# Kernel tuning notes

Hardware: AMD Instinct MI355X
Metric: run time of the kernel (lower is better)

## Reference

```python
import jax, jax.numpy as jnp
import numpy as np

B, S, D, H, V, N_SHARDS, CAP = 4, 512, 512, 8, 32000, 64, 128
HD = D // H


def _layernorm(x, g, b, eps=1e-5):
    mu = x.mean(-1, keepdims=True)
    var = ((x - mu) ** 2).mean(-1, keepdims=True)
    return (x - mu) * jax.lax.rsqrt(var + eps) * g + b


def setup_inputs() -> dict:
    key = jax.random.key(0)
    ks = jax.random.split(key, 16)
    s = 0.02
    return {
        'input_ids': jax.random.randint(ks[0], (B, S), 0, V, dtype=jnp.int32),
        'emb': jax.random.normal(ks[1], (V, D), jnp.float32) * s,
        'Wq': jax.random.normal(ks[2], (D, D), jnp.float32) * s,
        'Wk': jax.random.normal(ks[3], (D, D), jnp.float32) * s,
        'Wv': jax.random.normal(ks[4], (D, D), jnp.float32) * s,
        'Wo': jax.random.normal(ks[5], (D, D), jnp.float32) * s,
        'ln_g': jnp.ones((D,), jnp.float32),
        'ln_b': jnp.zeros((D,), jnp.float32),
        'W_router': jax.random.normal(ks[6], (D, N_SHARDS), jnp.float32),
        'mem_keys': jax.random.normal(ks[7], (N_SHARDS, CAP, D), jnp.float32) * s,
        'mem_values': jax.random.normal(ks[8], (N_SHARDS, CAP, D), jnp.float32) * s,
        'Wg_c': jax.random.normal(ks[9], (D, D), jnp.float32) * s,
        'Wg_m': jax.random.normal(ks[10], (D, D), jnp.float32) * s,
        'bg': jnp.zeros((D,), jnp.float32),
        'Wd': jax.random.normal(ks[11], (D, V), jnp.float32) * s,
        'bd': jnp.zeros((V,), jnp.float32),
        'top_k': 4,
    }


def reference(input_ids, emb, Wq, Wk, Wv, Wo, ln_g, ln_b, W_router,
              mem_keys, mem_values, Wg_c, Wg_m, bg, Wd, bd, top_k):
    # --- encode_context: embedding + causal MHA block (ContextSynthesizer) ---
    x = emb[input_ids]                                   # [B,S,D]
    q = (x @ Wq).reshape(B, S, H, HD)
    k = (x @ Wk).reshape(B, S, H, HD)
    v = (x @ Wv).reshape(B, S, H, HD)
    att = jnp.einsum('bqhd,bkhd->bhqk', q, k) / jnp.sqrt(jnp.float32(HD))
    causal = jnp.tril(jnp.ones((S, S), bool))
    att = jnp.where(causal[None, None], att, jnp.finfo(att.dtype).min)
    att = jax.nn.softmax(att, axis=-1)
    o = jnp.einsum('bhqk,bkhd->bqhd', att, v).reshape(B, S, D) @ Wo
    ctx = _layernorm(x + o, ln_g, ln_b)                  # [B,S,D]

    # --- LSHRouter: hyperplane projection -> shard id per token ---
    routes = jnp.argmax(ctx @ W_router, axis=-1)         # [B,S] int

    # --- MemoryShardStore.query, batched: per-token routed shard top-k read ---
    keys_g = mem_keys[routes]                            # [B,S,CAP,D] irregular gather
    scores = jnp.einsum('bscd,bsd->bsc', keys_g, ctx)    # [B,S,CAP]
    top_v, top_i = jax.lax.top_k(scores, top_k)          # [B,S,k]
    w = jax.nn.softmax(top_v, axis=-1)
    vals = mem_values[routes[:, :, None], top_i]         # [B,S,k,D]
    memory_stream = jnp.einsum('bsk,bskd->bsd', w, vals)

    # --- GatedMemoryFusion ---
    gate = jax.nn.sigmoid(ctx @ Wg_c + memory_stream @ Wg_m + bg)
    fused = gate * ctx + (1.0 - gate) * memory_stream

    # --- decoder; payload bias is zero (store holds no sequence_chunk records) ---
    logits = fused @ Wd + bd                             # [B,S,V]
    return logits
```

## Files before the change

### kernel.cpp

```cpp
#include <hip/hip_runtime.h>

typedef unsigned short u16;
typedef float f32x4 __attribute__((ext_vector_type(4)));
typedef short short8 __attribute__((ext_vector_type(8)));
typedef __bf16 bf16x8 __attribute__((ext_vector_type(8)));

#define B_  4
#define S_  512
#define D_  512
#define H_  8
#define HD_ 64
#define V_  32000
#define NSHARD_ 64
#define CAP_ 128
#define TOK_ (B_ * S_)

__device__ __forceinline__ float bf2f(u16 u) { return __uint_as_float(((unsigned)u) << 16); }
__device__ __forceinline__ u16 f2bf(float f) {
  unsigned u = __float_as_uint(f);
  u += 0x7FFFu + ((u >> 16) & 1u);
  return (u16)(u >> 16);
}

__device__ __forceinline__ f32x4 mfma16(short8 a, short8 b, f32x4 c) {
  return __builtin_amdgcn_mfma_f32_16x16x32_bf16(
      __builtin_bit_cast(bf16x8, a), __builtin_bit_cast(bf16x8, b), c, 0, 0, 0);
}

__device__ __forceinline__ void load_lds16(const void* g, void* l) {
  __builtin_amdgcn_global_load_lds(
      (const __attribute__((address_space(1))) void*)g,
      (__attribute__((address_space(3))) void*)l, 16, 0, 0);
}

template<int NS, bool ACC, int OM, bool CKLIM>
__global__ __launch_bounds__(256) void gemm_bt(
    const u16* __restrict__ Ah, const u16* __restrict__ Al, int ldA, long sA1, long sA2,
    const u16* __restrict__ Bh, const u16* __restrict__ Bl, int ldB, long sB1, long sB2,
    void* __restrict__ C0, void* __restrict__ C1, int ldC, long sC1, long sC2,
    int K, int z2n, float alpha)
{
  __shared__ u16 AsH[64 * 64];
  __shared__ u16 BsH[64 * 64];
  __shared__ u16 AsL[(NS == 3) ? 64 * 64 : 8];
  __shared__ u16 BsL[(NS == 3) ? 64 * 64 : 8];

  const int n0 = blockIdx.x * 64;
  const int m0 = blockIdx.y * 64;

  const int z = blockIdx.z;
  const int z1 = z / z2n, z2 = z - z1 * z2n;
  const long baseA = (long)z1 * sA1 + (long)z2 * sA2;
  const long baseB = (long)z1 * sB1 + (long)z2 * sB2;
  const long baseC = (long)z1 * sC1 + (long)z2 * sC2;

  const int tid = threadIdx.x;
  const int lane = tid & 63;
  const int w = tid >> 6;
  const int wm = (w >> 1) * 32, wn = (w & 1) * 32;
  const int fr = lane & 15, kg = lane >> 4;

  const int srow = lane >> 3;
  const int schunk = (lane & 7) ^ srow;

  const u16* gAh = Ah + baseA + (long)(m0 + w * 16 + srow) * ldA + schunk * 8;
  const u16* gBh = Bh + baseB + (long)(n0 + w * 16 + srow) * ldB + schunk * 8;
  const u16* gAl = (NS == 3) ? (Al + baseA + (long)(m0 + w * 16 + srow) * ldA + schunk * 8) : nullptr;
  const u16* gBl = (NS == 3) ? (Bl + baseB + (long)(n0 + w * 16 + srow) * ldB + schunk * 8) : nullptr;
  u16* lAh = &AsH[(w * 16) * 64];
  u16* lBh = &BsH[(w * 16) * 64];
  u16* lAl = &AsL[(NS == 3) ? (w * 16) * 64 : 0];
  u16* lBl = &BsL[(NS == 3) ? (w * 16) * 64 : 0];

  const int kmax = CKLIM ? (m0 + 64) : K;

  f32x4 acc[2][2] = {};

  for (int k0 = 0; k0 < kmax; k0 += 64) {
    load_lds16(gAh + k0, lAh);
    load_lds16(gAh + k0 + 8 * ldA, lAh + 8 * 64);
    load_lds16(gBh + k0, lBh);
    load_lds16(gBh + k0 + 8 * ldB, lBh + 8 * 64);
    if (NS == 3) {
      load_lds16(gAl + k0, lAl);
      load_lds16(gAl + k0 + 8 * ldA, lAl + 8 * 64);
      load_lds16(gBl + k0, lBl);
      load_lds16(gBl + k0 + 8 * ldB, lBl + 8 * 64);
    }
    __syncthreads();

    short8 ah[2][2], bh[2][2], al[2][2], bl[2][2];
#pragma unroll
    for (int mi = 0; mi < 2; ++mi) {
      int row = wm + mi * 16 + fr;
#pragma unroll
      for (int ks = 0; ks < 2; ++ks) {
        int idx = row * 64 + ((ks * 32 + kg * 8) ^ ((fr & 7) << 3));
        ah[mi][ks] = *(const short8*)&AsH[idx];
        if (NS == 3) al[mi][ks] = *(const short8*)&AsL[idx];
      }
    }
#pragma unroll
    for (int ni = 0; ni < 2; ++ni) {
      int row = wn + ni * 16 + fr;
#pragma unroll
      for (int ks = 0; ks < 2; ++ks) {
        int idx = row * 64 + ((ks * 32 + kg * 8) ^ ((fr & 7) << 3));
        bh[ni][ks] = *(const short8*)&BsH[idx];
        if (NS == 3) bl[ni][ks] = *(const short8*)&BsL[idx];
      }
    }
#pragma unroll
    for (int ks = 0; ks < 2; ++ks)
#pragma unroll
      for (int mi = 0; mi < 2; ++mi)
#pragma unroll
        for (int ni = 0; ni < 2; ++ni) {
          acc[mi][ni] = mfma16(ah[mi][ks], bh[ni][ks], acc[mi][ni]);
          if (NS == 3) {
            acc[mi][ni] = mfma16(ah[mi][ks], bl[ni][ks], acc[mi][ni]);
            acc[mi][ni] = mfma16(al[mi][ks], bh[ni][ks], acc[mi][ni]);
          }
        }
    __syncthreads();
  }

#pragma unroll
  for (int mi = 0; mi < 2; ++mi)
#pragma unroll
    for (int ni = 0; ni < 2; ++ni) {
      int gnc = n0 + wn + ni * 16 + fr;
#pragma unroll
      for (int r = 0; r < 4; ++r) {
        int gm = m0 + wm + mi * 16 + kg * 4 + r;
        float v = acc[mi][ni][r] * alpha;
        long idx = baseC + (long)gm * ldC + gnc;
        if (OM == 0) {
          float* C = (float*)C0;
          C[idx] = ACC ? (C[idx] + v) : v;
        } else {
          u16 h = f2bf(v);
          ((u16*)C0)[idx] = h;
          ((u16*)C1)[idx] = f2bf(v - bf2f(h));
        }
      }
    }
}

__global__ __launch_bounds__(256) void gate_gemm_k(
    const u16* __restrict__ Ah, const u16* __restrict__ Bh,
    const float* __restrict__ bgp, const float* __restrict__ ctxf,
    const float* __restrict__ msf, u16* __restrict__ fused)
{
  __shared__ u16 AsH[64 * 64];
  __shared__ u16 BsH[64 * 64];

  const int n0 = blockIdx.x * 64;
  const int m0 = blockIdx.y * 64;
  const int tid = threadIdx.x;
  const int lane = tid & 63;
  const int w = tid >> 6;
  const int wm = (w >> 1) * 32, wn = (w & 1) * 32;
  const int fr = lane & 15, kg = lane >> 4;
  const int srow = lane >> 3;
  const int schunk = (lane & 7) ^ srow;

  const u16* gAh = Ah + (long)(m0 + w * 16 + srow) * 1024 + schunk * 8;
  const u16* gBh = Bh + (long)(n0 + w * 16 + srow) * 1024 + schunk * 8;
  u16* lAh = &AsH[(w * 16) * 64];
  u16* lBh = &BsH[(w * 16) * 64];

  f32x4 acc[2][2] = {};

  for (int k0 = 0; k0 < 1024; k0 += 64) {
    load_lds16(gAh + k0, lAh);
    load_lds16(gAh + k0 + 8 * 1024, lAh + 8 * 64);
    load_lds16(gBh + k0, lBh);
    load_lds16(gBh + k0 + 8 * 1024, lBh + 8 * 64);
    __syncthreads();

    short8 ah[2][2], bh[2][2];
#pragma unroll
    for (int mi = 0; mi < 2; ++mi) {
      int row = wm + mi * 16 + fr;
#pragma unroll
      for (int ks = 0; ks < 2; ++ks)
        ah[mi][ks] = *(const short8*)&AsH[row * 64 +
                         ((ks * 32 + kg * 8) ^ ((fr & 7) << 3))];
    }
#pragma unroll
    for (int ni = 0; ni < 2; ++ni) {
      int row = wn + ni * 16 + fr;
#pragma unroll
      for (int ks = 0; ks < 2; ++ks)
        bh[ni][ks] = *(const short8*)&BsH[row * 64 +
                         ((ks * 32 + kg * 8) ^ ((fr & 7) << 3))];
    }
#pragma unroll
    for (int ks = 0; ks < 2; ++ks)
#pragma unroll
      for (int mi = 0; mi < 2; ++mi)
#pragma unroll
        for (int ni = 0; ni < 2; ++ni)
          acc[mi][ni] = mfma16(ah[mi][ks], bh[ni][ks], acc[mi][ni]);
    __syncthreads();
  }

#pragma unroll
  for (int mi = 0; mi < 2; ++mi)
#pragma unroll
    for (int ni = 0; ni < 2; ++ni) {
      int gnc = n0 + wn + ni * 16 + fr;
      float bv = bgp[gnc];
#pragma unroll
      for (int r = 0; r < 4; ++r) {
        int gm = m0 + wm + mi * 16 + kg * 4 + r;
        long idx = (long)gm * D_ + gnc;
        float g = 1.f / (1.f + expf(-(acc[mi][ni][r] + bv)));
        fused[idx] = f2bf(g * ctxf[idx] + (1.f - g) * msf[idx]);
      }
    }
}

__global__ __launch_bounds__(256) void qkt_k(
    const u16* __restrict__ qkvh, const u16* __restrict__ qkvl,
    float* __restrict__ att)
{
  const int n0 = blockIdx.x * 64;
  const int m0 = blockIdx.y * 64;
  if (n0 > m0 + 63) return;
  const int z = blockIdx.z;
  const int b = z >> 3, h = z & 7;
  const long qbase = (long)b * 512 * 1536 + h * 64;
  const long kbase = qbase + 512;
  const long cbase = (long)z * 512 * 512;

  const int tid = threadIdx.x;
  const int lane = tid & 63;
  const int w = tid >> 6;
  const int wm = (w >> 1) * 32, wn = (w & 1) * 32;
  const int fr = lane & 15, kg = lane >> 4;

  short8 ah[2][2], al[2][2], bh[2][2], bl[2][2];
#pragma unroll
  for (int mi = 0; mi < 2; ++mi)
#pragma unroll
    for (int ks = 0; ks < 2; ++ks) {
      long ra = qbase + (long)(m0 + wm + mi * 16 + fr) * 1536 + ks * 32 + kg * 8;
      ah[mi][ks] = *(const short8*)(qkvh + ra);
      al[mi][ks] = *(const short8*)(qkvl + ra);
    }
#pragma unroll
  for (int ni = 0; ni < 2; ++ni)
#pragma unroll
    for (int ks = 0; ks < 2; ++ks) {
      long rb = kbase + (long)(n0 + wn + ni * 16 + fr) * 1536 + ks * 32 + kg * 8;
      bh[ni][ks] = *(const short8*)(qkvh + rb);
      bl[ni][ks] = *(const short8*)(qkvl + rb);
    }

  f32x4 acc[2][2] = {};
#pragma unroll
  for (int ks = 0; ks < 2; ++ks)
#pragma unroll
    for (int mi = 0; mi < 2; ++mi)
#pragma unroll
      for (int ni = 0; ni < 2; ++ni) {
        acc[mi][ni] = mfma16(ah[mi][ks], bh[ni][ks], acc[mi][ni]);
        acc[mi][ni] = mfma16(ah[mi][ks], bl[ni][ks], acc[mi][ni]);
        acc[mi][ni] = mfma16(al[mi][ks], bh[ni][ks], acc[mi][ni]);
      }

#pragma unroll
  for (int mi = 0; mi < 2; ++mi)
#pragma unroll
    for (int ni = 0; ni < 2; ++ni) {
      int gnc = n0 + wn + ni * 16 + fr;
#pragma unroll
      for (int r = 0; r < 4; ++r) {
        int gm = m0 + wm + mi * 16 + kg * 4 + r;
        att[cbase + (long)gm * 512 + gnc] = acc[mi][ni][r] * 0.125f;
      }
    }
}

__global__ __launch_bounds__(512, 4) void logits_gemm_bk32_k(
    const u16* __restrict__ A, const u16* __restrict__ Bt,
    const float* __restrict__ bias, float* __restrict__ C)
{
  __shared__ u16 As[2][256 * 32];
  __shared__ u16 Bs[2][128 * 32];

  const int id = blockIdx.x;
  const int swz = (id & 7) * 250 + (id >> 3);
  const int m0 = (swz & 7) * 256;
  const int n0 = (swz >> 3) * 128;

  const int tid = threadIdx.x;
  const int lane = tid & 63;
  const int wid = tid >> 6;
  const int wr = wid >> 1;
  const int wc = wid & 1;
  const int fr = lane & 15, kg = lane >> 4;
  const int srow = lane >> 2;
  const int schunk = (lane & 3) ^ (srow & 3);

  f32x4 acc[4][4] = {};
  short8 a[4], b[4];

  auto stage = [&](int kt) {
    const int buf = kt & 1;
    const long kc = (long)kt * 32 + schunk * 8;
    load_lds16(A + (long)(m0 + wid * 16 + srow) * D_ + kc,
               &As[buf][(wid * 16) * 32]);
    load_lds16(A + (long)(m0 + 128 + wid * 16 + srow) * D_ + kc,
               &As[buf][(128 + wid * 16) * 32]);
    load_lds16(Bt + (long)(n0 + wid * 16 + srow) * D_ + kc,
               &Bs[buf][(wid * 16) * 32]);
  };
  auto readfrags = [&](int buf) {
#pragma unroll
    for (int mi = 0; mi < 4; ++mi) {
      int row = wr * 64 + mi * 16 + fr;
      a[mi] = *(const short8*)&As[buf][row * 32 + ((kg ^ (row & 3)) * 8)];
    }
#pragma unroll
    for (int ni = 0; ni < 4; ++ni) {
      int row = wc * 64 + ni * 16 + fr;
      b[ni] = *(const short8*)&Bs[buf][row * 32 + ((kg ^ (row & 3)) * 8)];
    }
  };

  stage(0);
  stage(1);

  for (int t = 0; t < 16; ++t) {
    __builtin_amdgcn_sched_barrier(0);
    if (t < 15) { asm volatile("s_waitcnt vmcnt(3)" ::: "memory"); }
    else        { asm volatile("s_waitcnt vmcnt(0)" ::: "memory"); }
    __builtin_amdgcn_s_barrier();
    __builtin_amdgcn_sched_barrier(0);

    readfrags(t & 1);
    asm volatile("s_waitcnt lgkmcnt(0)" ::: "memory");
    __builtin_amdgcn_sched_barrier(0);
    __builtin_amdgcn_s_barrier();
    __builtin_amdgcn_sched_barrier(0);

    if (t + 2 < 16) stage(t + 2);

    __builtin_amdgcn_sched_barrier(0);
    __builtin_amdgcn_s_setprio(1);
#pragma unroll
    for (int mi = 0; mi < 4; ++mi)
#pragma unroll
      for (int ni = 0; ni < 4; ++ni)
        acc[mi][ni] = mfma16(a[mi], b[ni], acc[mi][ni]);
    __builtin_amdgcn_s_setprio(0);
    __builtin_amdgcn_sched_barrier(0);
  }

#pragma unroll
  for (int ni = 0; ni < 4; ++ni) {
    int gnc = n0 + wc * 64 + ni * 16 + fr;
    float bv = bias[gnc];
#pragma unroll
    for (int mi = 0; mi < 4; ++mi)
#pragma unroll
      for (int r = 0; r < 4; ++r) {
        int gm = m0 + wr * 64 + mi * 16 + kg * 4 + r;
        __builtin_nontemporal_store(acc[mi][ni][r] + bv, &C[(long)gm * V_ + gnc]);
      }
  }
}

__global__ __launch_bounds__(256) void prep_weights_k(
    const float* __restrict__ Wq, const float* __restrict__ Wk,
    const float* __restrict__ Wv, const float* __restrict__ Wo,
    const float* __restrict__ Wgc, const float* __restrict__ Wgm,
    const float* __restrict__ Wd,
    u16* __restrict__ wqkvTh, u16* __restrict__ wqkvTl,
    u16* __restrict__ woTh, u16* __restrict__ woTl,
    u16* __restrict__ wgT, u16* __restrict__ wdT)
{
  const int bid = blockIdx.x;
  const float* W; u16 *oh, *ol = nullptr;
  int ldw, ldo, koff = 0, nb, kb;
  bool LO = false;
  if (bid < 384) {
    const int w = bid >> 6, tt = bid & 63;
    nb = tt & 7; kb = tt >> 3;
    ldw = 512; ldo = 512;
    switch (w) {
      case 0: W = Wq;  oh = wqkvTh;               ol = wqkvTl;               LO = true; break;
      case 1: W = Wk;  oh = wqkvTh + 512 * 512;   ol = wqkvTl + 512 * 512;   LO = true; break;
      case 2: W = Wv;  oh = wqkvTh + 2 * 512 * 512; ol = wqkvTl + 2 * 512 * 512; LO = true; break;
      case 3: W = Wo;  oh = woTh;                 ol = woTl;                 LO = true; break;
      case 4: W = Wgc; oh = wgT; ldo = 1024; break;
      default: W = Wgm; oh = wgT; ldo = 1024; koff = 512; break;
    }
  } else {
    const int tt = bid - 384;
    nb = tt % 500; kb = tt / 500;
    W = Wd; ldw = V_; ldo = 512; oh = wdT;
  }
  const int n0 = nb * 64, k0 = kb * 64;
  const int tid = threadIdx.x;
  __shared__ float t[64][65];
  {
    const int kk = tid >> 4;
    const int c4 = (tid & 15) * 4;
#pragma unroll
    for (int i = 0; i < 4; ++i) {
      f32x4 v = *(const f32x4*)(W + (long)(k0 + kk + i * 16) * ldw + n0 + c4);
      t[kk + i * 16][c4] = v[0];
      t[kk + i * 16][c4 + 1] = v[1];
      t[kk + i * 16][c4 + 2] = v[2];
      t[kk + i * 16][c4 + 3] = v[3];
    }
  }
  __syncthreads();
  {
    const int chunk = tid & 7;
    const int nn = tid >> 3;
#pragma unroll
    for (int j = 0; j < 2; ++j) {
      int n = nn + j * 32;
      u16 hbuf[8], lbuf[8];
#pragma unroll
      for (int e = 0; e < 8; ++e) {
        float fv = t[chunk * 8 + e][n];
        u16 h = f2bf(fv);
        hbuf[e] = h;
        lbuf[e] = f2bf(fv - bf2f(h));
      }
      long ob = (long)(n0 + n) * ldo + koff + k0 + chunk * 8;
      *(short8*)(oh + ob) = *(short8*)hbuf;
      if (LO) *(short8*)(ol + ob) = *(short8*)lbuf;
    }
  }
}

__global__ __launch_bounds__(256) void v_transpose_k(
    const u16* __restrict__ qh, const u16* __restrict__ ql,
    u16* __restrict__ vTh, u16* __restrict__ vTl)
{
  __shared__ u16 th[64][68];
  __shared__ u16 tl[64][68];
  const int z = blockIdx.y;
  const int b = z >> 3, h = z & 7;
  const int s0 = blockIdx.x * 64;
  const long ibase = ((long)(b * 512 + s0)) * 1536 + 1024 + h * 64;
  const int tid = threadIdx.x;
  {
    const int sr = tid >> 2;
    const int c8 = (tid & 3) * 16;
    const long src = ibase + (long)sr * 1536 + c8;
    *(short8*)&th[sr][c8]     = *(const short8*)(qh + src);
    *(short8*)&th[sr][c8 + 8] = *(const short8*)(qh + src + 8);
    *(short8*)&tl[sr][c8]     = *(const short8*)(ql + src);
    *(short8*)&tl[sr][c8 + 8] = *(const short8*)(ql + src + 8);
  }
  __syncthreads();
  {
    const int dr = tid >> 2;
    const int s8 = (tid & 3) * 16;
    u16 oh[16], ol[16];
#pragma unroll
    for (int j = 0; j < 16; ++j) { oh[j] = th[s8 + j][dr]; ol[j] = tl[s8 + j][dr]; }
    long ob = (long)z * 64 * 512 + (long)dr * 512 + s0 + s8;
    *(short8*)(vTh + ob)     = *(short8*)&oh[0];
    *(short8*)(vTh + ob + 8) = *(short8*)&oh[8];
    *(short8*)(vTl + ob)     = *(short8*)&ol[0];
    *(short8*)(vTl + ob + 8) = *(short8*)&ol[8];
  }
}

__global__ __launch_bounds__(128) void embed_k(const int* __restrict__ ids,
                                               const float* __restrict__ emb,
                                               float* __restrict__ x,
                                               u16* __restrict__ xh,
                                               u16* __restrict__ xl) {
  const int t = blockIdx.x;
  const long id = ids[t];
  const int c = threadIdx.x * 4;
  f32x4 v = *(const f32x4*)(emb + id * (long)D_ + c);
  *(f32x4*)(x + (long)t * D_ + c) = v;
  u16 hh[4], ll[4];
#pragma unroll
  for (int j = 0; j < 4; ++j) {
    u16 h = f2bf(v[j]);
    hh[j] = h;
    ll[j] = f2bf(v[j] - bf2f(h));
  }
  *(unsigned long long*)(xh + (long)t * D_ + c) = *(unsigned long long*)hh;
  *(unsigned long long*)(xl + (long)t * D_ + c) = *(unsigned long long*)ll;
}

__global__ __launch_bounds__(64) void softmax_causal_k(
    const float* __restrict__ att, u16* __restrict__ ph, u16* __restrict__ pl) {
  const int row = blockIdx.x;
  const int i = row & 511;
  const long base = (long)row << 9;
  const float* p = att + base;
  const int lane = threadIdx.x;
  const int c0 = lane * 8;
  float v[8];
  float m = -3.4e38f;
  if (c0 <= i) {
    f32x4 a = *(const f32x4*)(p + c0);
    f32x4 b2 = *(const f32x4*)(p + c0 + 4);
#pragma unroll
    for (int j = 0; j < 8; ++j) {
      float x = (j < 4) ? a[j] : b2[j - 4];
      x = (c0 + j <= i) ? x : -3.4e38f;
      v[j] = x;
      m = fmaxf(m, x);
    }
  } else {
#pragma unroll
    for (int j = 0; j < 8; ++j) v[j] = 0.f;
  }
#pragma unroll
  for (int off = 32; off; off >>= 1) m = fmaxf(m, __shfl_xor(m, off));
  float s = 0.f;
  if (c0 <= i) {
#pragma unroll
    for (int j = 0; j < 8; ++j) {
      float e = (c0 + j <= i) ? expf(v[j] - m) : 0.f;
      v[j] = e;
      s += e;
    }
  }
#pragma unroll
  for (int off = 32; off; off >>= 1) s += __shfl_xor(s, off);
  float inv = 1.f / s;
  if (c0 <= (i | 63)) {
    u16 hh[8], ll[8];
#pragma unroll
    for (int j = 0; j < 8; ++j) {
      float e = (c0 <= i) ? v[j] * inv : 0.f;
      u16 h = f2bf(e);
      hh[j] = h;
      ll[j] = f2bf(e - bf2f(h));
    }
    *(short8*)(ph + base + c0) = *(short8*)hh;
    *(short8*)(pl + base + c0) = *(short8*)ll;
  }
}

__global__ __launch_bounds__(128) void ln_route_k(
    const float* __restrict__ x, const float* __restrict__ proj,
    const float* __restrict__ g, const float* __restrict__ b,
    const float* __restrict__ Wr, const float* __restrict__ keys,
    const float* __restrict__ valsm,
    float* __restrict__ ctxf, u16* __restrict__ catA, float* __restrict__ msf)
{
  const int t = blockIdx.x;
  const int tid = threadIdx.x;
  __shared__ float sctx[D_];
  __shared__ float red2[4];
  __shared__ float spart[CAP_];
  __shared__ float sred2[2][64];
  __shared__ int s_route;
  __shared__ int sidx[4];
  __shared__ float sw[4];

  const int c = tid * 4;
  f32x4 xv = *(const f32x4*)(x + (long)t * D_ + c);
  f32x4 pv = *(const f32x4*)(proj + (long)t * D_ + c);
  float v0 = xv[0] + pv[0], v1 = xv[1] + pv[1];
  float v2 = xv[2] + pv[2], v3 = xv[3] + pv[3];
  float s = v0 + v1 + v2 + v3;
  float q = v0 * v0 + v1 * v1 + v2 * v2 + v3 * v3;
#pragma unroll
  for (int off = 32; off; off >>= 1) { s += __shfl_xor(s, off); q += __shfl_xor(q, off); }
  const int wave = tid >> 6, lane = tid & 63;
  if (lane == 0) { red2[wave] = s; red2[2 + wave] = q; }
  __syncthreads();
  s = red2[0] + red2[1];
  q = red2[2] + red2[3];
  float mu = s * (1.f / 512.f);
  float var = q * (1.f / 512.f) - mu * mu;
  float rs = rsqrtf(var + 1e-5f);
  f32x4 gv = *(const f32x4*)(g + c);
  f32x4 bv = *(const f32x4*)(b + c);
  f32x4 of;
  of[0] = (v0 - mu) * rs * gv[0] + bv[0];
  of[1] = (v1 - mu) * rs * gv[1] + bv[1];
  of[2] = (v2 - mu) * rs * gv[2] + bv[2];
  of[3] = (v3 - mu) * rs * gv[3] + bv[3];
  *(f32x4*)(ctxf + (long)t * D_ + c) = of;
  ((f32x4*)sctx)[tid] = of;
  {
    u16 hh[4];
#pragma unroll
    for (int j = 0; j < 4; ++j) hh[j] = f2bf(of[j]);
    *(unsigned long long*)(catA + (long)t * 1024 + c) = *(unsigned long long*)hh;
  }
  __syncthreads();

  {
    const int cc = tid & 63, half = tid >> 6;
    float accr = 0.f;
    const float* cp = sctx + half * 256;
    const float* wp = Wr + (long)(half * 256) * NSHARD_ + cc;
    for (int d = 0; d < 256; ++d) accr += cp[d] * wp[(long)d * NSHARD_];
    sred2[half][cc] = accr;
  }
  __syncthreads();
  if (tid < 64) {
    float v = sred2[0][tid] + sred2[1][tid];
    int idx = tid;
#pragma unroll
    for (int off = 32; off; off >>= 1) {
      float ov = __shfl_xor(v, off);
      int oi = __shfl_xor(idx, off);
      if (ov > v || (ov == v && oi < idx)) { v = ov; idx = oi; }
    }
    if (tid == 0) s_route = idx;
  }
  __syncthreads();
  const int route = s_route;

  {
    const float* krow = keys + ((long)route * CAP_ + tid) * D_;
    float sc = 0.f;
    for (int d0 = 0; d0 < D_; d0 += 4) {
      f32x4 kv = *(const f32x4*)(krow + d0);
      sc += sctx[d0] * kv[0] + sctx[d0 + 1] * kv[1] +
            sctx[d0 + 2] * kv[2] + sctx[d0 + 3] * kv[3];
    }
    spart[tid] = sc;
  }
  __syncthreads();

  for (int rep = 0; rep < 4; ++rep) {
    if (tid < 64) {
      float v1r = spart[tid]; int i1 = tid;
      float v2r = spart[tid + 64]; int i2 = tid + 64;
      float v; int idx;
      if (v2r > v1r) { v = v2r; idx = i2; } else { v = v1r; idx = i1; }
#pragma unroll
      for (int off = 32; off; off >>= 1) {
        float ov = __shfl_xor(v, off);
        int oi = __shfl_xor(idx, off);
        if (ov > v || (ov == v && oi < idx)) { v = ov; idx = oi; }
      }
      if (tid == 0) { sidx[rep] = idx; sw[rep] = v; spart[idx] = -3.4e38f; }
    }
    __syncthreads();
  }

  float w0 = sw[0], w1 = sw[1], w2 = sw[2], w3 = sw[3];
  float mx = fmaxf(fmaxf(w0, w1), fmaxf(w2, w3));
  float e0 = expf(w0 - mx), e1 = expf(w1 - mx), e2 = expf(w2 - mx), e3 = expf(w3 - mx);
  float inv = 1.f / (e0 + e1 + e2 + e3);
  float wk[4] = {e0 * inv, e1 * inv, e2 * inv, e3 * inv};

  float a0 = 0, a1 = 0, a2 = 0, a3 = 0;
#pragma unroll
  for (int k = 0; k < 4; ++k) {
    const float* vr = valsm + ((long)route * CAP_ + sidx[k]) * D_ + c;
    f32x4 vv = *(const f32x4*)vr;
    float w = wk[k];
    a0 += w * vv[0]; a1 += w * vv[1]; a2 += w * vv[2]; a3 += w * vv[3];
  }
  f32x4 om; om[0] = a0; om[1] = a1; om[2] = a2; om[3] = a3;
  *(f32x4*)(msf + (long)t * D_ + c) = om;
  u16 oh[4];
  oh[0] = f2bf(a0); oh[1] = f2bf(a1); oh[2] = f2bf(a2); oh[3] = f2bf(a3);
  *(unsigned long long*)(catA + (long)t * 1024 + 512 + c) =
      *(unsigned long long*)oh;
}

extern "C" void kernel_launch(void* const* d_in, const int* in_sizes, int n_in,
                              void* d_out, int out_size, void* d_ws, size_t ws_size,
                              hipStream_t stream) {
  const int*   ids  = (const int*)d_in[0];
  const float* emb  = (const float*)d_in[1];
  const float* Wq   = (const float*)d_in[2];
  const float* Wk   = (const float*)d_in[3];
  const float* Wv   = (const float*)d_in[4];
  const float* Wo   = (const float*)d_in[5];
  const float* ln_g = (const float*)d_in[6];
  const float* ln_b = (const float*)d_in[7];
  const float* Wr   = (const float*)d_in[8];
  const float* mk   = (const float*)d_in[9];
  const float* mv   = (const float*)d_in[10];
  const float* Wgc  = (const float*)d_in[11];
  const float* Wgm  = (const float*)d_in[12];
  const float* bg   = (const float*)d_in[13];
  const float* Wd   = (const float*)d_in[14];
  const float* bd   = (const float*)d_in[15];
  float* out = (float*)d_out;

  char* ws = (char*)d_ws;
  size_t off = 0;
  auto alloc = [&](size_t bytes) -> void* {
    void* p = ws + off;
    off += (bytes + 255) & ~(size_t)255;
    return p;
  };
  float* x      = (float*)alloc((size_t)TOK_ * D_ * 4);
  u16*   xh     = (u16*)  alloc((size_t)TOK_ * D_ * 2);
  u16*   xl     = (u16*)  alloc((size_t)TOK_ * D_ * 2);
  u16*   wqkvTh = (u16*)  alloc((size_t)3 * D_ * D_ * 2);
  u16*   wqkvTl = (u16*)  alloc((size_t)3 * D_ * D_ * 2);
  u16*   woTh   = (u16*)  alloc((size_t)D_ * D_ * 2);
  u16*   woTl   = (u16*)  alloc((size_t)D_ * D_ * 2);
  u16*   wgT    = (u16*)  alloc((size_t)D_ * 1024 * 2);
  u16*   wdT    = (u16*)  alloc((size_t)D_ * V_ * 2);
  u16*   qkvh   = (u16*)  alloc((size_t)TOK_ * 3 * D_ * 2);
  u16*   qkvl   = (u16*)  alloc((size_t)TOK_ * 3 * D_ * 2);
  u16*   vTh    = (u16*)  alloc((size_t)B_ * H_ * HD_ * S_ * 2);
  u16*   vTl    = (u16*)  alloc((size_t)B_ * H_ * HD_ * S_ * 2);
  float* att    = (float*)alloc((size_t)B_ * H_ * S_ * S_ * 4);
  u16*   ph     = (u16*)  alloc((size_t)B_ * H_ * S_ * S_ * 2);
  u16*   pl     = (u16*)  alloc((size_t)B_ * H_ * S_ * S_ * 2);
  u16*   oh     = (u16*)  alloc((size_t)TOK_ * D_ * 2);
  u16*   ol     = (u16*)  alloc((size_t)TOK_ * D_ * 2);
  float* proj   = (float*)alloc((size_t)TOK_ * D_ * 4);
  float* ctxf   = (float*)alloc((size_t)TOK_ * D_ * 4);
  u16*   catA   = (u16*)  alloc((size_t)TOK_ * 1024 * 2);
  float* msf    = (float*)alloc((size_t)TOK_ * D_ * 4);
  u16*   fused  = (u16*)  alloc((size_t)TOK_ * D_ * 2);

  prep_weights_k<<<4384, 256, 0, stream>>>(
      Wq, Wk, Wv, Wo, Wgc, Wgm, Wd,
      wqkvTh, wqkvTl, woTh, woTl, wgT, wdT);

  embed_k<<<TOK_, 128, 0, stream>>>(ids, emb, x, xh, xl);

  {
    dim3 g(1536 / 64, TOK_ / 64, 1);
    gemm_bt<3, false, 1, false><<<g, 256, 0, stream>>>(
        xh, xl, D_, 0, 0, wqkvTh, wqkvTl, D_, 0, 0,
        qkvh, qkvl, 1536, 0, 0, D_, 1, 1.f);
  }

  {
    dim3 g(S_ / 64, B_ * H_, 1);
    v_transpose_k<<<g, 256, 0, stream>>>(qkvh, qkvl, vTh, vTl);
  }

  {
    dim3 g(S_ / 64, S_ / 64, B_ * H_);
    qkt_k<<<g, 256, 0, stream>>>(qkvh, qkvl, att);
  }

  softmax_causal_k<<<B_ * H_ * S_, 64, 0, stream>>>(att, ph, pl);

  {
    dim3 g(1, S_ / 64, B_ * H_);
    gemm_bt<3, false, 1, true><<<g, 256, 0, stream>>>(
        ph, pl, S_, (long)H_ * S_ * S_, (long)S_ * S_,
        vTh, vTl, S_, (long)H_ * HD_ * S_, (long)HD_ * S_,
        oh, ol, D_, (long)S_ * D_, HD_,
        S_, H_, 1.f);
  }

  {
    dim3 g(D_ / 64, TOK_ / 64, 1);
    gemm_bt<3, false, 0, false><<<g, 256, 0, stream>>>(
        oh, ol, D_, 0, 0, woTh, woTl, D_, 0, 0,
        proj, nullptr, D_, 0, 0, D_, 1, 1.f);
  }

  ln_route_k<<<TOK_, 128, 0, stream>>>(
      x, proj, ln_g, ln_b, Wr, mk, mv, ctxf, catA, msf);

  {
    dim3 g(D_ / 64, TOK_ / 64, 1);
    gate_gemm_k<<<g, 256, 0, stream>>>(catA, wgT, bg, ctxf, msf, fused);
  }

  logits_gemm_bk32_k<<<2000, 512, 0, stream>>>(fused, wdT, bd, out);
}
```

Baseline: 299.3 us.

## Fuse embedding into weight prep and overlap Wd transpose with QK^T kernel

Merges the embedding gather into the small weight-prep kernel, moves the large Wd transpose/bf16 conversion into extra blocks of the QK^T launch, and drops the fp32 copy of x by reconstructing it from the hi/lo bf16 split in the layernorm kernel. The intent is to cut launches, remove an fp32 write and read of x, and let the memory-bound Wd conversion run alongside the mostly idle causal QK^T grid. The risk is heterogeneous blocks unbalancing the grid, plus a tiny precision change from rebuilding x out of two bf16 halves.

Result: faster. 289.7 us (-3.2%).

```diff
diff --git a/kernel.cpp b/kernel.cpp
--- a/kernel.cpp
+++ b/kernel.cpp
@@ -4,6 +4,7 @@
 typedef float f32x4 __attribute__((ext_vector_type(4)));
 typedef short short8 __attribute__((ext_vector_type(8)));
 typedef __bf16 bf16x8 __attribute__((ext_vector_type(8)));
+typedef unsigned long long ull;
 
 #define B_  4
 #define S_  512
@@ -147,6 +148,104 @@
     }
 }
 
+__global__ __launch_bounds__(256) void qkt_wd_k(
+    const u16* __restrict__ qkvh, const u16* __restrict__ qkvl,
+    float* __restrict__ att,
+    const float* __restrict__ Wd, u16* __restrict__ wdT)
+{
+  __shared__ float t[64][65];
+  const int z = blockIdx.z;
+  const int tid = threadIdx.x;
+
+  if (z >= 32) {
+    const int tt = (z - 32) * 64 + blockIdx.y * 8 + blockIdx.x;
+    if (tt >= 4000) return;
+    const int nb = tt % 500, kb = tt / 500;
+    const int n0 = nb * 64, k0 = kb * 64;
+    {
+      const int kk = tid >> 4;
+      const int c4 = (tid & 15) * 4;
+#pragma unroll
+      for (int i = 0; i < 4; ++i) {
+        f32x4 v = *(const f32x4*)(Wd + (long)(k0 + kk + i * 16) * V_ + n0 + c4);
+        t[kk + i * 16][c4] = v[0];
+        t[kk + i * 16][c4 + 1] = v[1];
+        t[kk + i * 16][c4 + 2] = v[2];
+        t[kk + i * 16][c4 + 3] = v[3];
+      }
+    }
+    __syncthreads();
+    {
+      const int chunk = tid & 7;
+      const int nn = tid >> 3;
+#pragma unroll
+      for (int j = 0; j < 2; ++j) {
+        int n = nn + j * 32;
+        u16 hbuf[8];
+#pragma unroll
+        for (int e = 0; e < 8; ++e) hbuf[e] = f2bf(t[chunk * 8 + e][n]);
+        *(short8*)(wdT + (long)(n0 + n) * 512 + k0 + chunk * 8) = *(short8*)hbuf;
+      }
+    }
+    return;
+  }
+
+  const int n0 = blockIdx.x * 64;
+  const int m0 = blockIdx.y * 64;
+  if (n0 > m0 + 63) return;
+  const int b = z >> 3, h = z & 7;
+  const long qbase = (long)b * 512 * 1536 + h * 64;
+  const long kbase = qbase + 512;
+  const long cbase = (long)z * 512 * 512;
+
+  const int lane = tid & 63;
+  const int w = tid >> 6;
+  const int wm = (w >> 1) * 32, wn = (w & 1) * 32;
+  const int fr = lane & 15, kg = lane >> 4;
+
+  short8 ah[2][2], al[2][2], bh[2][2], bl[2][2];
+#pragma unroll
+  for (int mi = 0; mi < 2; ++mi)
+#pragma unroll
+    for (int ks = 0; ks < 2; ++ks) {
+      long ra = qbase + (long)(m0 + wm + mi * 16 + fr) * 1536 + ks * 32 + kg * 8;
+      ah[mi][ks] = *(const short8*)(qkvh + ra);
+      al[mi][ks] = *(const short8*)(qkvl + ra);
+    }
+#pragma unroll
+  for (int ni = 0; ni < 2; ++ni)
+#pragma unroll
+    for (int ks = 0; ks < 2; ++ks) {
+      long rb = kbase + (long)(n0 + wn + ni * 16 + fr) * 1536 + ks * 32 + kg * 8;
+      bh[ni][ks] = *(const short8*)(qkvh + rb);
+      bl[ni][ks] = *(const short8*)(qkvl + rb);
+    }
+
+  f32x4 acc[2][2] = {};
+#pragma unroll
+  for (int ks = 0; ks < 2; ++ks)
+#pragma unroll
+    for (int mi = 0; mi < 2; ++mi)
+#pragma unroll
+      for (int ni = 0; ni < 2; ++ni) {
+        acc[mi][ni] = mfma16(ah[mi][ks], bh[ni][ks], acc[mi][ni]);
+        acc[mi][ni] = mfma16(ah[mi][ks], bl[ni][ks], acc[mi][ni]);
+        acc[mi][ni] = mfma16(al[mi][ks], bh[ni][ks], acc[mi][ni]);
+      }
+
+#pragma unroll
+  for (int mi = 0; mi < 2; ++mi)
+#pragma unroll
+    for (int ni = 0; ni < 2; ++ni) {
+      int gnc = n0 + wn + ni * 16 + fr;
+#pragma unroll
+      for (int r = 0; r < 4; ++r) {
+        int gm = m0 + wm + mi * 16 + kg * 4 + r;
+        att[cbase + (long)gm * 512 + gnc] = acc[mi][ni][r] * 0.125f;
+      }
+    }
+}
+
 __global__ __launch_bounds__(256) void gate_gemm_k(
     const u16* __restrict__ Ah, const u16* __restrict__ Bh,
     const float* __restrict__ bgp, const float* __restrict__ ctxf,
@@ -218,68 +317,6 @@
         long idx = (long)gm * D_ + gnc;
         float g = 1.f / (1.f + expf(-(acc[mi][ni][r] + bv)));
         fused[idx] = f2bf(g * ctxf[idx] + (1.f - g) * msf[idx]);
-      }
-    }
-}
-
-__global__ __launch_bounds__(256) void qkt_k(
-    const u16* __restrict__ qkvh, const u16* __restrict__ qkvl,
-    float* __restrict__ att)
-{
-  const int n0 = blockIdx.x * 64;
-  const int m0 = blockIdx.y * 64;
-  if (n0 > m0 + 63) return;
-  const int z = blockIdx.z;
-  const int b = z >> 3, h = z & 7;
-  const long qbase = (long)b * 512 * 1536 + h * 64;
-  const long kbase = qbase + 512;
-  const long cbase = (long)z * 512 * 512;
-
-  const int tid = threadIdx.x;
-  const int lane = tid & 63;
-  const int w = tid >> 6;
-  const int wm = (w >> 1) * 32, wn = (w & 1) * 32;
-  const int fr = lane & 15, kg = lane >> 4;
-
-  short8 ah[2][2], al[2][2], bh[2][2], bl[2][2];
-#pragma unroll
-  for (int mi = 0; mi < 2; ++mi)
-#pragma unroll
-    for (int ks = 0; ks < 2; ++ks) {
-      long ra = qbase + (long)(m0 + wm + mi * 16 + fr) * 1536 + ks * 32 + kg * 8;
-      ah[mi][ks] = *(const short8*)(qkvh + ra);
-      al[mi][ks] = *(const short8*)(qkvl + ra);
-    }
-#pragma unroll
-  for (int ni = 0; ni < 2; ++ni)
-#pragma unroll
-    for (int ks = 0; ks < 2; ++ks) {
-      long rb = kbase + (long)(n0 + wn + ni * 16 + fr) * 1536 + ks * 32 + kg * 8;
-      bh[ni][ks] = *(const short8*)(qkvh + rb);
-      bl[ni][ks] = *(const short8*)(qkvl + rb);
-    }
-
-  f32x4 acc[2][2] = {};
-#pragma unroll
-  for (int ks = 0; ks < 2; ++ks)
-#pragma unroll
-    for (int mi = 0; mi < 2; ++mi)
-#pragma unroll
-      for (int ni = 0; ni < 2; ++ni) {
-        acc[mi][ni] = mfma16(ah[mi][ks], bh[ni][ks], acc[mi][ni]);
-        acc[mi][ni] = mfma16(ah[mi][ks], bl[ni][ks], acc[mi][ni]);
-        acc[mi][ni] = mfma16(al[mi][ks], bh[ni][ks], acc[mi][ni]);
-      }
-
-#pragma unroll
-  for (int mi = 0; mi < 2; ++mi)
-#pragma unroll
-    for (int ni = 0; ni < 2; ++ni) {
-      int gnc = n0 + wn + ni * 16 + fr;
-#pragma unroll
-      for (int r = 0; r < 4; ++r) {
-        int gm = m0 + wm + mi * 16 + kg * 4 + r;
-        att[cbase + (long)gm * 512 + gnc] = acc[mi][ni][r] * 0.125f;
       }
     }
 }
@@ -374,45 +411,57 @@
   }
 }
 
-__global__ __launch_bounds__(256) void prep_weights_k(
+__global__ __launch_bounds__(256) void prep_embed_k(
     const float* __restrict__ Wq, const float* __restrict__ Wk,
     const float* __restrict__ Wv, const float* __restrict__ Wo,
     const float* __restrict__ Wgc, const float* __restrict__ Wgm,
-    const float* __restrict__ Wd,
     u16* __restrict__ wqkvTh, u16* __restrict__ wqkvTl,
     u16* __restrict__ woTh, u16* __restrict__ woTl,
-    u16* __restrict__ wgT, u16* __restrict__ wdT)
+    u16* __restrict__ wgT,
+    const int* __restrict__ ids, const float* __restrict__ emb,
+    u16* __restrict__ xh, u16* __restrict__ xl)
 {
   const int bid = blockIdx.x;
+  const int tid = threadIdx.x;
+
+  if (bid >= 384) {
+    const int t = (bid - 384) * 2 + (tid >> 7);
+    const int c = (tid & 127) * 4;
+    const long id = ids[t];
+    f32x4 v = *(const f32x4*)(emb + id * (long)D_ + c);
+    u16 hh[4], ll[4];
+#pragma unroll
+    for (int j = 0; j < 4; ++j) {
+      u16 h = f2bf(v[j]);
+      hh[j] = h;
+      ll[j] = f2bf(v[j] - bf2f(h));
+    }
+    *(ull*)(xh + (long)t * D_ + c) = *(ull*)hh;
+    *(ull*)(xl + (long)t * D_ + c) = *(ull*)ll;
+    return;
+  }
+
   const float* W; u16 *oh, *ol = nullptr;
-  int ldw, ldo, koff = 0, nb, kb;
+  int ldo = 512, koff = 0;
   bool LO = false;
-  if (bid < 384) {
-    const int w = bid >> 6, tt = bid & 63;
-    nb = tt & 7; kb = tt >> 3;
-    ldw = 512; ldo = 512;
-    switch (w) {
-      case 0: W = Wq;  oh = wqkvTh;               ol = wqkvTl;               LO = true; break;
-      case 1: W = Wk;  oh = wqkvTh + 512 * 512;   ol = wqkvTl + 512 * 512;   LO = true; break;
-      case 2: W = Wv;  oh = wqkvTh + 2 * 512 * 512; ol = wqkvTl + 2 * 512 * 512; LO = true; break;
-      case 3: W = Wo;  oh = woTh;                 ol = woTl;                 LO = true; break;
-      case 4: W = Wgc; oh = wgT; ldo = 1024; break;
-      default: W = Wgm; oh = wgT; ldo = 1024; koff = 512; break;
-    }
-  } else {
-    const int tt = bid - 384;
-    nb = tt % 500; kb = tt / 500;
-    W = Wd; ldw = V_; ldo = 512; oh = wdT;
+  const int w = bid >> 6, tt = bid & 63;
+  const int nb = tt & 7, kb = tt >> 3;
+  switch (w) {
+    case 0: W = Wq;  oh = wqkvTh;                 ol = wqkvTl;                 LO = true; break;
+    case 1: W = Wk;  oh = wqkvTh + 512 * 512;     ol = wqkvTl + 512 * 512;     LO = true; break;
+    case 2: W = Wv;  oh = wqkvTh + 2 * 512 * 512; ol = wqkvTl + 2 * 512 * 512; LO = true; break;
+    case 3: W = Wo;  oh = woTh;                   ol = woTl;                   LO = true; break;
+    case 4: W = Wgc; oh = wgT; ldo = 1024; break;
+    default: W = Wgm; oh = wgT; ldo = 1024; koff = 512; break;
   }
   const int n0 = nb * 64, k0 = kb * 64;
-  const int tid = threadIdx.x;
   __shared__ float t[64][65];
   {
     const int kk = tid >> 4;
     const int c4 = (tid & 15) * 4;
 #pragma unroll
     for (int i = 0; i < 4; ++i) {
-      f32x4 v = *(const f32x4*)(W + (long)(k0 + kk + i * 16) * ldw + n0 + c4);
+      f32x4 v = *(const f32x4*)(W + (long)(k0 + kk + i * 16) * 512 + n0 + c4);
       t[kk + i * 16][c4] = v[0];
       t[kk + i * 16][c4 + 1] = v[1];
       t[kk + i * 16][c4 + 2] = v[2];
@@ -474,27 +523,6 @@
     *(short8*)(vTl + ob)     = *(short8*)&ol[0];
     *(short8*)(vTl + ob + 8) = *(short8*)&ol[8];
   }
-}
-
-__global__ __launch_bounds__(128) void embed_k(const int* __restrict__ ids,
-                                               const float* __restrict__ emb,
-                                               float* __restrict__ x,
-                                               u16* __restrict__ xh,
-                                               u16* __restrict__ xl) {
-  const int t = blockIdx.x;
-  const long id = ids[t];
-  const int c = threadIdx.x * 4;
-  f32x4 v = *(const f32x4*)(emb + id * (long)D_ + c);
-  *(f32x4*)(x + (long)t * D_ + c) = v;
-  u16 hh[4], ll[4];
-#pragma unroll
-  for (int j = 0; j < 4; ++j) {
-    u16 h = f2bf(v[j]);
-    hh[j] = h;
-    ll[j] = f2bf(v[j] - bf2f(h));
-  }
-  *(unsigned long long*)(xh + (long)t * D_ + c) = *(unsigned long long*)hh;
-  *(unsigned long long*)(xl + (long)t * D_ + c) = *(unsigned long long*)ll;
 }
 
 __global__ __launch_bounds__(64) void softmax_causal_k(
@@ -550,7 +578,8 @@
 }
 
 __global__ __launch_bounds__(128) void ln_route_k(
-    const float* __restrict__ x, const float* __restrict__ proj,
+    const u16* __restrict__ xh, const u16* __restrict__ xl,
+    const float* __restrict__ proj,
     const float* __restrict__ g, const float* __restrict__ b,
     const float* __restrict__ Wr, const float* __restrict__ keys,
     const float* __restrict__ valsm,
@@ -567,10 +596,13 @@
   __shared__ float sw[4];
 
   const int c = tid * 4;
-  f32x4 xv = *(const f32x4*)(x + (long)t * D_ + c);
+  ull hv = *(const ull*)(xh + (long)t * D_ + c);
+  ull lv = *(const ull*)(xl + (long)t * D_ + c);
   f32x4 pv = *(const f32x4*)(proj + (long)t * D_ + c);
-  float v0 = xv[0] + pv[0], v1 = xv[1] + pv[1];
-  float v2 = xv[2] + pv[2], v3 = xv[3] + pv[3];
+  float v0 = bf2f((u16)(hv)) + bf2f((u16)(lv)) + pv[0];
+  float v1 = bf2f((u16)(hv >> 16)) + bf2f((u16)(lv >> 16)) + pv[1];
+  float v2 = bf2f((u16)(hv >> 32)) + bf2f((u16)(lv >> 32)) + pv[2];
+  float v3 = bf2f((u16)(hv >> 48)) + bf2f((u16)(lv >> 48)) + pv[3];
   float s = v0 + v1 + v2 + v3;
   float q = v0 * v0 + v1 * v1 + v2 * v2 + v3 * v3;
 #pragma unroll
@@ -596,7 +628,7 @@
     u16 hh[4];
 #pragma unroll
     for (int j = 0; j < 4; ++j) hh[j] = f2bf(of[j]);
-    *(unsigned long long*)(catA + (long)t * 1024 + c) = *(unsigned long long*)hh;
+    *(ull*)(catA + (long)t * 1024 + c) = *(ull*)hh;
   }
   __syncthreads();
 
@@ -668,10 +700,9 @@
   }
   f32x4 om; om[0] = a0; om[1] = a1; om[2] = a2; om[3] = a3;
   *(f32x4*)(msf + (long)t * D_ + c) = om;
-  u16 oh[4];
-  oh[0] = f2bf(a0); oh[1] = f2bf(a1); oh[2] = f2bf(a2); oh[3] = f2bf(a3);
-  *(unsigned long long*)(catA + (long)t * 1024 + 512 + c) =
-      *(unsigned long long*)oh;
+  u16 ohh[4];
+  ohh[0] = f2bf(a0); ohh[1] = f2bf(a1); ohh[2] = f2bf(a2); ohh[3] = f2bf(a3);
+  *(ull*)(catA + (long)t * 1024 + 512 + c) = *(ull*)ohh;
 }
 
 extern "C" void kernel_launch(void* const* d_in, const int* in_sizes, int n_in,
@@ -702,7 +733,6 @@
     off += (bytes + 255) & ~(size_t)255;
     return p;
   };
-  float* x      = (float*)alloc((size_t)TOK_ * D_ * 4);
   u16*   xh     = (u16*)  alloc((size_t)TOK_ * D_ * 2);
   u16*   xl     = (u16*)  alloc((size_t)TOK_ * D_ * 2);
   u16*   wqkvTh = (u16*)  alloc((size_t)3 * D_ * D_ * 2);
@@ -726,11 +756,13 @@
   float* msf    = (float*)alloc((size_t)TOK_ * D_ * 4);
   u16*   fused  = (u16*)  alloc((size_t)TOK_ * D_ * 2);
 
-  prep_weights_k<<<4384, 256, 0, stream>>>(
-      Wq, Wk, Wv, Wo, Wgc, Wgm, Wd,
-      wqkvTh, wqkvTl, woTh, woTl, wgT, wdT);
-
-  embed_k<<<TOK_, 128, 0, stream>>>(ids, emb, x, xh, xl);
+  const long SD  = (long)S_ * D_;
+  const long SSq = (long)S_ * S_;
+  const long HSS = (long)H_ * S_ * S_;
+
+  prep_embed_k<<<1408, 256, 0, stream>>>(
+      Wq, Wk, Wv, Wo, Wgc, Wgm,
+      wqkvTh, wqkvTl, woTh, woTl, wgT, ids, emb, xh, xl);
 
   {
     dim3 g(1536 / 64, TOK_ / 64, 1);
@@ -745,8 +777,8 @@
   }
 
   {
-    dim3 g(S_ / 64, S_ / 64, B_ * H_);
-    qkt_k<<<g, 256, 0, stream>>>(qkvh, qkvl, att);
+    dim3 g(8, 8, 32 + 63);
+    qkt_wd_k<<<g, 256, 0, stream>>>(qkvh, qkvl, att, Wd, wdT);
   }
 
   softmax_causal_k<<<B_ * H_ * S_, 64, 0, stream>>>(att, ph, pl);
@@ -754,9 +786,9 @@
   {
     dim3 g(1, S_ / 64, B_ * H_);
     gemm_bt<3, false, 1, true><<<g, 256, 0, stream>>>(
-        ph, pl, S_, (long)H_ * S_ * S_, (long)S_ * S_,
+        ph, pl, S_, HSS, SSq,
         vTh, vTl, S_, (long)H_ * HD_ * S_, (long)HD_ * S_,
-        oh, ol, D_, (long)S_ * D_, HD_,
+        oh, ol, D_, SD, HD_,
         S_, H_, 1.f);
   }
 
@@ -768,7 +800,7 @@
   }
 
   ln_route_k<<<TOK_, 128, 0, stream>>>(
-      x, proj, ln_g, ln_b, Wr, mk, mv, ctxf, catA, msf);
+      xh, xl, proj, ln_g, ln_b, Wr, mk, mv, ctxf, catA, msf);
 
   {
     dim3 g(D_ / 64, TOK_ / 64, 1);
```
